# Optimization experiments

Measured on AMD Instinct MI355X. Metric: run time of the kernel, lower is better.

The kernel has to match this reference:

```python
import jax, jax.numpy as jnp
import numpy as np

B, N, M, D, NH, HD = 2, 1024, 1024, 1536, 16, 96
RD = HD // 3  # per-axis rotary dim = 32
EPS = 1e-6
SCALE = HD ** -0.5


def _rmsnorm(y, w):
    return y * jax.lax.rsqrt(jnp.mean(y * y, axis=-1, keepdims=True) + EPS) * w


def _rope_tables(T, H, W):
    # inv_freqs identical for t/h/w since all three dims are RD
    inv_f = 1.0 / (10000.0 ** (jnp.arange(0, RD, 2, dtype=jnp.float32)[: RD // 2] / RD))
    gt, gh, gw = jnp.meshgrid(
        jnp.arange(T, dtype=jnp.float32),
        jnp.arange(H, dtype=jnp.float32),
        jnp.arange(W, dtype=jnp.float32),
        indexing='ij')
    ft = gt.reshape(-1, 1) * inv_f[None, :]  # [L, RD//2]
    fh = gh.reshape(-1, 1) * inv_f[None, :]
    fw = gw.reshape(-1, 1) * inv_f[None, :]
    return (jnp.cos(ft), jnp.sin(ft), jnp.cos(fh), jnp.sin(fh), jnp.cos(fw), jnp.sin(fw))


def _apply_rope(xq, cos, sin):
    # xq: [B, L, NH, RD]; cos/sin: [L, RD//2]
    c = jnp.concatenate([cos, cos], axis=-1)[None, :, None, :]
    s = jnp.concatenate([sin, sin], axis=-1)[None, :, None, :]
    x1, x2 = jnp.split(xq, 2, axis=-1)
    rot = jnp.concatenate([-x2, x1], axis=-1)
    return xq * c + rot * s


def setup_inputs() -> dict:
    key = jax.random.key(0)
    ks = jax.random.split(key, 10)
    w = lambda k: jax.random.normal(k, (D, D), dtype=jnp.float32) * 0.02
    return {
        'cond': jax.random.normal(ks[0], (B, N, D), dtype=jnp.float32),
        'x': jax.random.normal(ks[1], (B, M, D), dtype=jnp.float32),
        'cond_q_w': w(ks[2]), 'cond_k_w': w(ks[3]), 'cond_v_w': w(ks[4]),
        'cond_qnorm_w': jnp.ones((D,), jnp.float32),
        'cond_knorm_w': jnp.ones((D,), jnp.float32),
        'cond_proj_w': w(ks[5]),
        'x_q_w': w(ks[6]), 'x_k_w': w(ks[7]), 'x_v_w': w(ks[8]),
        'x_qnorm_w': jnp.ones((D,), jnp.float32),
        'x_knorm_w': jnp.ones((D,), jnp.float32),
        'x_proj_w': w(ks[9]),
        'T': 2, 'H': 32, 'W': 32,
    }


def reference(cond, x, cond_q_w, cond_k_w, cond_v_w, cond_qnorm_w, cond_knorm_w,
              cond_proj_w, x_q_w, x_k_w, x_v_w, x_qnorm_w, x_knorm_w, x_proj_w,
              T, H, W):
    # dual-stream QKV + RMSNorm (qkv_bias=False, eval -> no dropout)
    cq = _rmsnorm(cond @ cond_q_w, cond_qnorm_w).reshape(B, N, NH, HD)
    ck = _rmsnorm(cond @ cond_k_w, cond_knorm_w).reshape(B, N, NH, HD)
    cv = (cond @ cond_v_w).reshape(B, N, NH, HD)
    xq = _rmsnorm(x @ x_q_w, x_qnorm_w).reshape(B, M, NH, HD)
    xk = _rmsnorm(x @ x_k_w, x_knorm_w).reshape(B, M, NH, HD)
    xv = (x @ x_v_w).reshape(B, M, NH, HD)

    q = jnp.concatenate([cq, xq], axis=1)  # [B, N+M, NH, HD]
    k = jnp.concatenate([ck, xk], axis=1)
    v = jnp.concatenate([cv, xv], axis=1)

    # 3D RoPE: split head_dim into t/h/w thirds and rotate each with its own freqs
    cos_t, sin_t, cos_h, sin_h, cos_w, sin_w = _rope_tables(T, H, W)
    qt, qh, qw = jnp.split(q, 3, axis=-1)
    kt, kh, kw = jnp.split(k, 3, axis=-1)
    q = jnp.concatenate([_apply_rope(qt, cos_t, sin_t),
                         _apply_rope(qh, cos_h, sin_h),
                         _apply_rope(qw, cos_w, sin_w)], axis=-1)
    k = jnp.concatenate([_apply_rope(kt, cos_t, sin_t),
                         _apply_rope(kh, cos_h, sin_h),
                         _apply_rope(kw, cos_w, sin_w)], axis=-1)

    # joint non-causal SDPA
    scores = jnp.einsum('blhd,bmhd->bhlm', q, k) * SCALE
    attn = jax.nn.softmax(scores, axis=-1)
    out = jnp.einsum('bhlm,bmhd->blhd', attn, v).reshape(B, N + M, D)

    cond_out = out[:, :N] @ cond_proj_w
    x_out = out[:, N:] @ x_proj_w
    return cond_out, x_out
```

## Files before the change

### kernel.cpp

```cpp
#include <hip/hip_runtime.h>
#include <stdint.h>

#define DEV __device__ __forceinline__

using f32x4  = __attribute__((ext_vector_type(4))) float;
using f32x16 = __attribute__((ext_vector_type(16))) float;
using bf16x8 = __attribute__((ext_vector_type(8))) short;

DEV ushort f2bf(float f){
  uint32_t u = __float_as_uint(f);
  u += 0x7FFFu + ((u >> 16) & 1u);
  return (ushort)(u >> 16);
}
DEV float bf2f(ushort h){ return __uint_as_float(((uint32_t)h) << 16); }

DEV void async16(const void* g, void* l){
  __builtin_amdgcn_global_load_lds(
      (const __attribute__((address_space(1))) void*)g,
      (__attribute__((address_space(3))) void*)l, 16, 0, 0);
}

DEV int swz32(int d, int row){ return (d & ~31) | ((((d >> 3) ^ row) & 3) << 3) | (d & 7); }

union FU { uint4 u; bf16x8 v; };
DEV bf16x8 as_bf16x8(uint a, uint b, uint c, uint d){ FU f; f.u = make_uint4(a,b,c,d); return f.v; }

__global__ __launch_bounds__(256) void k_conv_in(const float* __restrict__ src, ushort* __restrict__ dst){
  int i = (blockIdx.x * 256 + threadIdx.x) * 4;
  int row = i / 1536;
  int d = i - row * 1536;
  float4 v = *(const float4*)(src + i);
  ushort4 o;
  o.x = f2bf(v.x); o.y = f2bf(v.y); o.z = f2bf(v.z); o.w = f2bf(v.w);
  *(ushort4*)(dst + (size_t)row * 1536 + swz32(d, row)) = o;
}

__global__ __launch_bounds__(256) void k_transpose_w(
    const float* w0, const float* w1, const float* w2, const float* w3,
    const float* w4, const float* w5, const float* w6, const float* w7,
    ushort* __restrict__ dst){
  __shared__ float tile[32][33];
  int z = blockIdx.z;
  const float* src = (z==0)?w0:(z==1)?w1:(z==2)?w2:(z==3)?w3:(z==4)?w4:(z==5)?w5:(z==6)?w6:w7;
  int n0 = blockIdx.x * 32;
  int k0 = blockIdx.y * 32;
  int tx = threadIdx.x;
  int ty = threadIdx.y;
  for (int j = 0; j < 4; ++j)
    tile[ty + j*8][tx] = src[(size_t)(k0 + ty + j*8) * 1536 + n0 + tx];
  __syncthreads();
  ushort* d = dst + (size_t)z * 1536 * 1536;
  for (int j = 0; j < 4; ++j){
    int n = n0 + ty + j*8;
    int k = k0 + tx;
    d[(size_t)n * 1536 + swz32(k, n)] = f2bf(tile[tx][ty + j*8]);
  }
}

template<bool OUT_BF16>
DEV void gemm_tile(const ushort* __restrict__ A, const ushort* __restrict__ Bt, void* __restrict__ Cp,
                   int K, int lda, int ldb, int ldc, int m0, int n0){
  __shared__ ushort As[4096];
  __shared__ ushort Bs[4096];
  int tid = threadIdx.x;
  int w = tid >> 6, lane = tid & 63;
  int g = lane >> 4, fr = lane & 15;
  int wm = (w >> 1) * 64, wn = (w & 1) * 64;
  int co = ((g ^ fr) & 3) * 8;
  f32x4 acc[4][4] = {};
  for (int kt = 0; kt < K; kt += 32){
    __syncthreads();
#pragma unroll
    for (int i = 0; i < 2; ++i){
      int c = i * 256 + tid;
      int row = c >> 2, seg = c & 3;
      async16(A  + (size_t)(m0 + row) * lda + kt + seg * 8, As + (i*256 + w*64) * 8);
      async16(Bt + (size_t)(n0 + row) * ldb + kt + seg * 8, Bs + (i*256 + w*64) * 8);
    }
    __syncthreads();
    bf16x8 af[4], bf[4];
#pragma unroll
    for (int mi = 0; mi < 4; ++mi) af[mi] = *(const bf16x8*)(As + (wm + mi*16 + fr) * 32 + co);
#pragma unroll
    for (int ni = 0; ni < 4; ++ni) bf[ni] = *(const bf16x8*)(Bs + (wn + ni*16 + fr) * 32 + co);
#pragma unroll
    for (int mi = 0; mi < 4; ++mi)
#pragma unroll
      for (int ni = 0; ni < 4; ++ni)
        acc[mi][ni] = __builtin_amdgcn_mfma_f32_16x16x32_bf16(af[mi], bf[ni], acc[mi][ni], 0, 0, 0);
  }
  int cr = (lane >> 4) * 4, cc = lane & 15;
#pragma unroll
  for (int mi = 0; mi < 4; ++mi)
#pragma unroll
    for (int ni = 0; ni < 4; ++ni)
#pragma unroll
      for (int r = 0; r < 4; ++r){
        size_t idx = (size_t)(m0 + wm + mi*16 + cr + r) * ldc + (n0 + wn + ni*16 + cc);
        if (OUT_BF16) ((ushort*)Cp)[idx] = f2bf(acc[mi][ni][r]);
        else          ((float*)Cp)[idx]  = acc[mi][ni][r];
      }
}

__global__ __launch_bounds__(256) void k_gemm_qkv(const ushort* __restrict__ inb, const ushort* __restrict__ Wt,
                                                  ushort* __restrict__ Y){
  int f = blockIdx.x;
  int nid = (f & 7) * 144 + (f >> 3);
  int z = nid / 576; int rr = nid - z * 576;
  int by = rr / 36;  int bx = rr - by * 36;
  gemm_tile<true>(inb + (size_t)z * 2048 * 1536, Wt + (size_t)z * 4608 * 1536,
                  Y + (size_t)z * 2048 * 4608, 1536, 1536, 1536, 4608,
                  by * 128, bx * 128);
}

__global__ __launch_bounds__(256) void k_gemm_proj(const ushort* __restrict__ AO, const ushort* __restrict__ Wtp,
                                                   float* __restrict__ out){
  int f = blockIdx.x;
  int nid = (f & 7) * 48 + (f >> 3);
  int z = nid / 96; int rr = nid - z * 96;
  int by = rr / 12; int bx = rr - by * 12;
  int s = z >> 1, bb = z & 1;
  gemm_tile<false>(AO + (size_t)(bb*2048 + s*1024) * 1536, Wtp + (size_t)s * 1536 * 1536,
                   (void*)(out + (size_t)(s*2048 + bb*1024) * 1536), 1536, 1536, 1536, 1536,
                   by * 128, bx * 128);
}

__global__ __launch_bounds__(256) void k_norm_rope(
    const ushort* __restrict__ Y,
    const float* __restrict__ qn_c, const float* __restrict__ kn_c,
    const float* __restrict__ qn_x, const float* __restrict__ kn_x,
    ushort* __restrict__ Qb, ushort* __restrict__ Kb, ushort* __restrict__ Vb){
  int r = blockIdx.x;
  int z = blockIdx.y;
  const ushort* y = Y + ((size_t)z * 2048 + r) * 4608;
  const float* qw = z ? qn_x : qn_c;
  const float* kw = z ? kn_x : kn_c;
  int b = r >> 10;
  int l = (z << 10) + (r & 1023);
  int tid = threadIdx.x;
  __shared__ float cs[48], sn[48];
  if (tid < 48){
    int axis = tid >> 4, fj = tid & 15;
    int pos = (axis == 0) ? (l >> 10) : ((axis == 1) ? ((l >> 5) & 31) : (l & 31));
    float inv = __expf(-(float)fj * 0.5756462732485114f);
    float a = (float)pos * inv;
    sn[tid] = sinf(a); cs[tid] = cosf(a);
  }
  float yq1[3], yq2[3], yk1[3], yk2[3];
  float ssq = 0.f, ssk = 0.f;
#pragma unroll
  for (int i = 0; i < 3; ++i){
    int p = tid + i*256;
    int head = p / 48, rem = p % 48;
    int c1 = head*96 + (rem >> 4)*32 + (rem & 15);
    float a1 = bf2f(y[c1]),        a2 = bf2f(y[c1 + 16]);
    float b1 = bf2f(y[1536 + c1]), b2 = bf2f(y[1536 + c1 + 16]);
    yq1[i]=a1; yq2[i]=a2; yk1[i]=b1; yk2[i]=b2;
    ssq += a1*a1 + a2*a2;
    ssk += b1*b1 + b2*b2;
  }
#pragma unroll
  for (int mm = 1; mm < 64; mm <<= 1){
    ssq += __shfl_xor(ssq, mm);
    ssk += __shfl_xor(ssk, mm);
  }
  __shared__ float red[8];
  int w = tid >> 6;
  if ((tid & 63) == 0){ red[w] = ssq; red[4 + w] = ssk; }
  __syncthreads();
  float scq = rsqrtf((red[0]+red[1]+red[2]+red[3]) * (1.f/1536.f) + 1e-6f);
  float sck = rsqrtf((red[4]+red[5]+red[6]+red[7]) * (1.f/1536.f) + 1e-6f);
  float scqS = scq * 0.1020620726159658f;
#pragma unroll
  for (int i = 0; i < 3; ++i){
    int p = tid + i*256;
    int head = p / 48, rem = p % 48;
    int axis = rem >> 4, fj = rem & 15;
    int c1 = head*96 + axis*32 + fj;
    float c = cs[rem], s = sn[rem];
    size_t rowb = ((size_t)(b*16 + head) * 2048 + l) * 96;
    float a1 = yq1[i] * scqS * qw[c1], a2 = yq2[i] * scqS * qw[c1 + 16];
    Qb[rowb + axis*32 + fj]      = f2bf(a1*c - a2*s);
    Qb[rowb + axis*32 + fj + 16] = f2bf(a2*c + a1*s);
    float b1 = yk1[i] * sck * kw[c1], b2 = yk2[i] * sck * kw[c1 + 16];
    int d1 = axis*32 + fj;
    Kb[rowb + d1]      = f2bf(b1*c - b2*s);
    Kb[rowb + d1 + 16] = f2bf(b2*c + b1*s);
  }
#pragma unroll
  for (int i = 0; i < 6; ++i){
    int cidx = tid + i*256;
    int head = cidx / 96, hd = cidx - head*96;
    Vb[((size_t)(b*16 + head) * 2048 + l) * 96 + hd] = y[3072 + cidx];
  }
}

__global__ __launch_bounds__(256) void k_transpose_v(const ushort* __restrict__ V, ushort* __restrict__ Vt){
  __shared__ ushort t[32][33];
  int bh = blockIdx.z;
  const ushort* src = V + (size_t)bh * 2048 * 96;
  ushort* dst = Vt + (size_t)bh * 96 * 2048;
  int c0 = blockIdx.x * 32;
  int r0 = blockIdx.y * 32;
  int tx = threadIdx.x, ty = threadIdx.y;
  for (int j = 0; j < 4; ++j)
    t[ty + j*8][tx] = src[(size_t)(r0 + ty + j*8) * 96 + c0 + tx];
  __syncthreads();
  for (int j = 0; j < 4; ++j){
    int d = c0 + ty + j*8;
    int l = r0 + tx;
    dst[(size_t)d * 2048 + l] = t[tx][ty + j*8];
  }
}

__global__ __launch_bounds__(256, 2) void k_attn(const ushort* __restrict__ Qb, const ushort* __restrict__ Kb,
                                                 const ushort* __restrict__ Vt, ushort* __restrict__ AO){
  __shared__ ushort Ks[64*100];
  __shared__ ushort Vs[96*68];
  int id = blockIdx.x;
  int nid = (id & 7) * 64 + (id >> 3);
  int qt = nid & 15, bh = nid >> 4;
  int b = bh >> 4, head = bh & 15;
  const ushort* Qh = Qb + (size_t)bh * 2048 * 96;
  const ushort* Kh = Kb + (size_t)bh * 2048 * 96;
  const ushort* Vh = Vt + (size_t)bh * 96 * 2048;
  int tid = threadIdx.x;
  int w = tid >> 6, lane = tid & 63;
  int h = lane >> 5, c = lane & 31;
  int q0 = qt * 128 + w * 32;

  bf16x8 qf[6];
#pragma unroll
  for (int kb = 0; kb < 6; ++kb)
    qf[kb] = *(const bf16x8*)(Qh + (size_t)(q0 + c) * 96 + kb*16 + h*8);

  int gko[3], lko[3], gvo[3], lvo[3];
#pragma unroll
  for (int i = 0; i < 3; ++i){
    int fc = i*256 + tid;
    int krow = (fc * 683) >> 13;
    int kc8  = (fc - krow*12) * 8;
    gko[i] = krow*96 + kc8;
    lko[i] = krow*100 + kc8;
    int vrow = fc >> 3;
    int vc8  = (fc & 7) * 8;
    gvo[i] = vrow*2048 + vc8;
    lvo[i] = vrow*68 + (vc8 ^ ((vrow & 7) << 3));
  }
  uint4 kst[3], vst[3];
#pragma unroll
  for (int i = 0; i < 3; ++i){
    kst[i] = *(const uint4*)(Kh + gko[i]);
    vst[i] = *(const uint4*)(Vh + (size_t)gvo[i]);
  }

  f32x16 o[3] = {};
  float dpart = 0.f;

  for (int kt = 0; kt < 32; ++kt){
#pragma unroll
    for (int i = 0; i < 3; ++i){
      *(uint2*)(Ks + lko[i])     = make_uint2(kst[i].x, kst[i].y);
      *(uint2*)(Ks + lko[i] + 4) = make_uint2(kst[i].z, kst[i].w);
      *(uint2*)(Vs + lvo[i])     = make_uint2(vst[i].x, vst[i].y);
      *(uint2*)(Vs + lvo[i] + 4) = make_uint2(vst[i].z, vst[i].w);
    }
    if (kt + 1 < 32){
#pragma unroll
      for (int i = 0; i < 3; ++i){
        kst[i] = *(const uint4*)(Kh + (kt+1)*6144 + gko[i]);
        vst[i] = *(const uint4*)(Vh + (kt+1)*64 + (size_t)gvo[i]);
      }
    }
    asm volatile("s_waitcnt lgkmcnt(0)" ::: "memory");
    __builtin_amdgcn_s_barrier();
    asm volatile("" ::: "memory");

#pragma unroll
    for (int ni = 0; ni < 2; ++ni){
      f32x16 sa = {};
#pragma unroll
      for (int kb = 0; kb < 6; ++kb){
        const ushort* kp = Ks + (ni*32 + c)*100 + kb*16 + h*8;
        uint2 lo = *(const uint2*)kp;
        uint2 hi = *(const uint2*)(kp + 4);
        sa = __builtin_amdgcn_mfma_f32_32x32x16_bf16(as_bf16x8(lo.x, lo.y, hi.x, hi.y), qf[kb], sa, 0, 0, 0);
      }
      float p[16];
#pragma unroll
      for (int e = 0; e < 16; ++e){
        float x = fmaf(sa[e], 1.44269504f, -14.4269504f);
        asm("v_exp_f32 %0, %1" : "=v"(p[e]) : "v"(x));
      }
      dpart += (((p[0]+p[1])+(p[2]+p[3])) + ((p[4]+p[5])+(p[6]+p[7])))
             + (((p[8]+p[9])+(p[10]+p[11])) + ((p[12]+p[13])+(p[14]+p[15])));
      uint u[8];
#pragma unroll
      for (int e = 0; e < 8; ++e)
        asm("v_cvt_pk_bf16_f32 %0, %1, %2" : "=v"(u[e]) : "v"(p[2*e]), "v"(p[2*e+1]));
      asm("v_permlane32_swap_b32 %0, %1" : "+v"(u[0]), "+v"(u[2]));
      asm("v_permlane32_swap_b32 %0, %1" : "+v"(u[1]), "+v"(u[3]));
      asm("v_permlane32_swap_b32 %0, %1" : "+v"(u[4]), "+v"(u[6]));
      asm("v_permlane32_swap_b32 %0, %1" : "+v"(u[5]), "+v"(u[7]));
      bf16x8 pf0 = as_bf16x8(u[0], u[1], u[2], u[3]);
      bf16x8 pf1 = as_bf16x8(u[4], u[5], u[6], u[7]);
#pragma unroll
      for (int dt = 0; dt < 3; ++dt){
#pragma unroll
        for (int ks = 0; ks < 2; ++ks){
          int chunk = 4*ni + 2*ks + h;
          const ushort* vp = Vs + (dt*32 + c)*68 + ((chunk ^ (c & 7)) << 3);
          uint2 lo = *(const uint2*)vp;
          uint2 hi = *(const uint2*)(vp + 4);
          o[dt] = __builtin_amdgcn_mfma_f32_32x32x16_bf16(ks ? pf1 : pf0,
                    as_bf16x8(lo.x, lo.y, hi.x, hi.y), o[dt], 0, 0, 0);
        }
      }
    }
    asm volatile("" ::: "memory");
    __builtin_amdgcn_s_barrier();
    asm volatile("" ::: "memory");
  }

  float dtot = dpart + __shfl_xor(dpart, 32);
#pragma unroll
  for (int r = 0; r < 16; ++r){
    int qloc = (r & 3) + 8*(r >> 2) + 4*h;
    float den = __shfl(dtot, qloc);
    float dinv = __builtin_amdgcn_rcpf(den);
    size_t rowoff = ((size_t)b * 2048 + q0 + qloc) * 1536 + head * 96;
    int colsw = ((((c >> 3) ^ r) & 3) << 3) | (c & 7);
#pragma unroll
    for (int dt = 0; dt < 3; ++dt){
      float val = o[dt][r] * dinv;
      uint pk; asm("v_cvt_pk_bf16_f32 %0, %1, %2" : "=v"(pk) : "v"(val), "v"(val));
      AO[rowoff + dt*32 + colsw] = (ushort)pk;
    }
  }
}

extern "C" void kernel_launch(void* const* d_in, const int* in_sizes, int n_in,
                              void* d_out, int out_size, void* d_ws, size_t ws_size,
                              hipStream_t stream){
  const float* cond = (const float*)d_in[0];
  const float* x    = (const float*)d_in[1];
  const float* wq_c = (const float*)d_in[2];
  const float* wk_c = (const float*)d_in[3];
  const float* wv_c = (const float*)d_in[4];
  const float* qn_c = (const float*)d_in[5];
  const float* kn_c = (const float*)d_in[6];
  const float* wp_c = (const float*)d_in[7];
  const float* wq_x = (const float*)d_in[8];
  const float* wk_x = (const float*)d_in[9];
  const float* wv_x = (const float*)d_in[10];
  const float* qn_x = (const float*)d_in[11];
  const float* kn_x = (const float*)d_in[12];
  const float* wp_x = (const float*)d_in[13];

  char* ws = (char*)d_ws;
  ushort* inb = (ushort*)(ws);
  ushort* Wt  = (ushort*)(ws + 12582912ll);
  ushort* Y   = (ushort*)(ws + 50331648ll);
  ushort* Vt  = (ushort*)(ws + 50331648ll);
  ushort* Qb  = (ushort*)(ws + 88080384ll);
  ushort* Kb  = (ushort*)(ws + 100663296ll);
  ushort* Vb  = (ushort*)(ws + 113246208ll);
  ushort* AO  = inb;

  k_conv_in<<<3072, 256, 0, stream>>>(cond, inb);
  k_conv_in<<<3072, 256, 0, stream>>>(x, inb + 3145728);
  k_transpose_w<<<dim3(48,48,8), dim3(32,8), 0, stream>>>(wq_c, wk_c, wv_c, wq_x, wk_x, wv_x, wp_c, wp_x, Wt);
  k_gemm_qkv<<<1152, 256, 0, stream>>>(inb, Wt, Y);
  k_norm_rope<<<dim3(2048,2), 256, 0, stream>>>(Y, qn_c, kn_c, qn_x, kn_x, Qb, Kb, Vb);
  k_transpose_v<<<dim3(3,64,32), dim3(32,8), 0, stream>>>(Vb, Vt);
  k_attn<<<512, 256, 0, stream>>>(Qb, Kb, Vt, AO);
  k_gemm_proj<<<384, 256, 0, stream>>>(AO, Wt + (size_t)9216*1536, (float*)d_out);
  (void)in_sizes; (void)n_in; (void)out_size; (void)ws_size;
}
```

Before: 239.6 us.

## Drop global swizzle, use k-chunk-major LDS layout with BK=64 GEMM tiles

Removes the XOR swizzle from the global bf16 inputs, weights and attention output, and instead gives the GEMM LDS tiles a chunk-major layout (column chunk by row) so fragment reads stay free of bank conflicts without any swizzle. The GEMM K-step grows from 32 to 64, which doubles LDS tile size and halves the number of barriers per tile. The input conversion kernel now handles 8 elements per thread, and the attention MFMA sections are wrapped in s_setprio to favour matrix work across waves. The larger LDS footprint may reduce occupancy, and the global access pattern of the async loads changes.

```diff
diff --git a/kernel.cpp b/kernel.cpp
--- a/kernel.cpp
+++ b/kernel.cpp
@@ -20,19 +20,17 @@
       (__attribute__((address_space(3))) void*)l, 16, 0, 0);
 }
 
-DEV int swz32(int d, int row){ return (d & ~31) | ((((d >> 3) ^ row) & 3) << 3) | (d & 7); }
-
 union FU { uint4 u; bf16x8 v; };
 DEV bf16x8 as_bf16x8(uint a, uint b, uint c, uint d){ FU f; f.u = make_uint4(a,b,c,d); return f.v; }
 
 __global__ __launch_bounds__(256) void k_conv_in(const float* __restrict__ src, ushort* __restrict__ dst){
-  int i = (blockIdx.x * 256 + threadIdx.x) * 4;
-  int row = i / 1536;
-  int d = i - row * 1536;
-  float4 v = *(const float4*)(src + i);
-  ushort4 o;
-  o.x = f2bf(v.x); o.y = f2bf(v.y); o.z = f2bf(v.z); o.w = f2bf(v.w);
-  *(ushort4*)(dst + (size_t)row * 1536 + swz32(d, row)) = o;
+  int i = (blockIdx.x * 256 + threadIdx.x) * 8;
+  float4 a = *(const float4*)(src + i);
+  float4 b = *(const float4*)(src + i + 4);
+  union { ushort s[8]; uint4 q; } o;
+  o.s[0]=f2bf(a.x); o.s[1]=f2bf(a.y); o.s[2]=f2bf(a.z); o.s[3]=f2bf(a.w);
+  o.s[4]=f2bf(b.x); o.s[5]=f2bf(b.y); o.s[6]=f2bf(b.z); o.s[7]=f2bf(b.w);
+  *(uint4*)(dst + i) = o.q;
 }
 
 __global__ __launch_bounds__(256) void k_transpose_w(
@@ -53,50 +51,52 @@
   for (int j = 0; j < 4; ++j){
     int n = n0 + ty + j*8;
     int k = k0 + tx;
-    d[(size_t)n * 1536 + swz32(k, n)] = f2bf(tile[tx][ty + j*8]);
+    d[(size_t)n * 1536 + k] = f2bf(tile[tx][ty + j*8]);
   }
 }
 
 template<bool OUT_BF16>
 DEV void gemm_tile(const ushort* __restrict__ A, const ushort* __restrict__ Bt, void* __restrict__ Cp,
                    int K, int lda, int ldb, int ldc, int m0, int n0){
-  __shared__ ushort As[4096];
-  __shared__ ushort Bs[4096];
+  __shared__ ushort As[8192];
+  __shared__ ushort Bs[8192];
   int tid = threadIdx.x;
   int w = tid >> 6, lane = tid & 63;
   int g = lane >> 4, fr = lane & 15;
   int wm = (w >> 1) * 64, wn = (w & 1) * 64;
-  int co = ((g ^ fr) & 3) * 8;
   f32x4 acc[4][4] = {};
-  for (int kt = 0; kt < K; kt += 32){
+  for (int kt = 0; kt < K; kt += 64){
     __syncthreads();
 #pragma unroll
-    for (int i = 0; i < 2; ++i){
-      int c = i * 256 + tid;
-      int row = c >> 2, seg = c & 3;
-      async16(A  + (size_t)(m0 + row) * lda + kt + seg * 8, As + (i*256 + w*64) * 8);
-      async16(Bt + (size_t)(n0 + row) * ldb + kt + seg * 8, Bs + (i*256 + w*64) * 8);
+    for (int i = 0; i < 4; ++i){
+      int ci = i * 256 + tid;
+      int row = ci & 127, cc = ci >> 7;
+      async16(A  + (size_t)(m0 + row) * lda + kt + cc * 8, As + (i*256 + w*64) * 8);
+      async16(Bt + (size_t)(n0 + row) * ldb + kt + cc * 8, Bs + (i*256 + w*64) * 8);
     }
     __syncthreads();
-    bf16x8 af[4], bf[4];
-#pragma unroll
-    for (int mi = 0; mi < 4; ++mi) af[mi] = *(const bf16x8*)(As + (wm + mi*16 + fr) * 32 + co);
-#pragma unroll
-    for (int ni = 0; ni < 4; ++ni) bf[ni] = *(const bf16x8*)(Bs + (wn + ni*16 + fr) * 32 + co);
-#pragma unroll
-    for (int mi = 0; mi < 4; ++mi)
-#pragma unroll
-      for (int ni = 0; ni < 4; ++ni)
-        acc[mi][ni] = __builtin_amdgcn_mfma_f32_16x16x32_bf16(af[mi], bf[ni], acc[mi][ni], 0, 0, 0);
-  }
-  int cr = (lane >> 4) * 4, cc = lane & 15;
+#pragma unroll
+    for (int ks = 0; ks < 2; ++ks){
+      bf16x8 af[4], bf[4];
+#pragma unroll
+      for (int mi = 0; mi < 4; ++mi) af[mi] = *(const bf16x8*)(As + (((ks*4 + g)*128) + wm + mi*16 + fr) * 8);
+#pragma unroll
+      for (int ni = 0; ni < 4; ++ni) bf[ni] = *(const bf16x8*)(Bs + (((ks*4 + g)*128) + wn + ni*16 + fr) * 8);
+#pragma unroll
+      for (int mi = 0; mi < 4; ++mi)
+#pragma unroll
+        for (int ni = 0; ni < 4; ++ni)
+          acc[mi][ni] = __builtin_amdgcn_mfma_f32_16x16x32_bf16(af[mi], bf[ni], acc[mi][ni], 0, 0, 0);
+    }
+  }
+  int cr = (lane >> 4) * 4, cc2 = lane & 15;
 #pragma unroll
   for (int mi = 0; mi < 4; ++mi)
 #pragma unroll
     for (int ni = 0; ni < 4; ++ni)
 #pragma unroll
       for (int r = 0; r < 4; ++r){
-        size_t idx = (size_t)(m0 + wm + mi*16 + cr + r) * ldc + (n0 + wn + ni*16 + cc);
+        size_t idx = (size_t)(m0 + wm + mi*16 + cr + r) * ldc + (n0 + wn + ni*16 + cc2);
         if (OUT_BF16) ((ushort*)Cp)[idx] = f2bf(acc[mi][ni][r]);
         else          ((float*)Cp)[idx]  = acc[mi][ni][r];
       }
@@ -279,6 +279,7 @@
 #pragma unroll
     for (int ni = 0; ni < 2; ++ni){
       f32x16 sa = {};
+      __builtin_amdgcn_s_setprio(1);
 #pragma unroll
       for (int kb = 0; kb < 6; ++kb){
         const ushort* kp = Ks + (ni*32 + c)*100 + kb*16 + h*8;
@@ -286,6 +287,7 @@
         uint2 hi = *(const uint2*)(kp + 4);
         sa = __builtin_amdgcn_mfma_f32_32x32x16_bf16(as_bf16x8(lo.x, lo.y, hi.x, hi.y), qf[kb], sa, 0, 0, 0);
       }
+      __builtin_amdgcn_s_setprio(0);
       float p[16];
 #pragma unroll
       for (int e = 0; e < 16; ++e){
@@ -304,6 +306,7 @@
       asm("v_permlane32_swap_b32 %0, %1" : "+v"(u[5]), "+v"(u[7]));
       bf16x8 pf0 = as_bf16x8(u[0], u[1], u[2], u[3]);
       bf16x8 pf1 = as_bf16x8(u[4], u[5], u[6], u[7]);
+      __builtin_amdgcn_s_setprio(1);
 #pragma unroll
       for (int dt = 0; dt < 3; ++dt){
 #pragma unroll
@@ -316,6 +319,7 @@
                     as_bf16x8(lo.x, lo.y, hi.x, hi.y), o[dt], 0, 0, 0);
         }
       }
+      __builtin_amdgcn_s_setprio(0);
     }
     asm volatile("" ::: "memory");
     __builtin_amdgcn_s_barrier();
@@ -329,12 +333,11 @@
     float den = __shfl(dtot, qloc);
     float dinv = __builtin_amdgcn_rcpf(den);
     size_t rowoff = ((size_t)b * 2048 + q0 + qloc) * 1536 + head * 96;
-    int colsw = ((((c >> 3) ^ r) & 3) << 3) | (c & 7);
 #pragma unroll
     for (int dt = 0; dt < 3; ++dt){
       float val = o[dt][r] * dinv;
       uint pk; asm("v_cvt_pk_bf16_f32 %0, %1, %2" : "=v"(pk) : "v"(val), "v"(val));
-      AO[rowoff + dt*32 + colsw] = (ushort)pk;
+      AO[rowoff + dt*32 + c] = (ushort)pk;
     }
   }
 }
@@ -367,8 +370,8 @@
   ushort* Vb  = (ushort*)(ws + 113246208ll);
   ushort* AO  = inb;
 
-  k_conv_in<<<3072, 256, 0, stream>>>(cond, inb);
-  k_conv_in<<<3072, 256, 0, stream>>>(x, inb + 3145728);
+  k_conv_in<<<1536, 256, 0, stream>>>(cond, inb);
+  k_conv_in<<<1536, 256, 0, stream>>>(x, inb + 3145728);
   k_transpose_w<<<dim3(48,48,8), dim3(32,8), 0, stream>>>(wq_c, wk_c, wv_c, wq_x, wk_x, wv_x, wp_c, wp_x, Wt);
   k_gemm_qkv<<<1152, 256, 0, stream>>>(inb, Wt, Y);
   k_norm_rope<<<dim3(2048,2), 256, 0, stream>>>(Y, qn_c, kn_c, qn_x, kn_x, Qb, Kb, Vb);
```

Measured after the change: 318.0 us. +32.7%, slower.
